# Kernel tuning notes

Measured on AMD Instinct MI355X. Metric: run time of the kernel, lower is better.

## Reference

```python
import jax, jax.numpy as jnp
import numpy as np

TEMPERATURE = 0.1  # base_temperature=0.07 is unused in the original forward
K = 100            # hard-coded top-k in the original forward


def setup_inputs() -> dict:
    key = jax.random.key(0)
    k1, k2, k3, k4 = jax.random.split(key, 4)
    B, T, D, N = 16, 2048, 256, 128
    context_feature = jax.random.normal(k1, (B, T, D), dtype=jnp.float32)
    target_feature = jax.random.normal(k2, (B, T, D), dtype=jnp.float32)
    # torch.unique(mask_index): supply a pre-uniqued sorted 1D index set directly
    mask_index = jnp.sort(jax.random.permutation(k3, T)[:N]).astype(jnp.int32)
    phone_label = jax.random.randint(k4, (B, T), 0, 100, dtype=jnp.int32)
    return {"context_feature": context_feature, "target_feature": target_feature,
            "mask_index": mask_index, "phone_label": phone_label}


def reference(context_feature, target_feature, mask_index, phone_label):
    B, T, D = context_feature.shape
    N = mask_index.shape[0]

    # phone gather + inequality mask (BN, BT)
    phone_n = phone_label[:, mask_index].reshape(B * N)
    phone_t = phone_label.reshape(B * T)
    neq_mask = (phone_n[:, None] != phone_t[None, :]).astype(context_feature.dtype)

    anchors = context_feature[:, mask_index, :].reshape(B * N, D)
    negative = target_feature.reshape(B * T, D)
    positive = target_feature[:, mask_index, :].reshape(B * N, D)

    a_norm = jnp.linalg.norm(anchors, axis=1)   # (BN,)
    p_norm = jnp.linalg.norm(positive, axis=1)  # (BN,)
    n_norm = jnp.linalg.norm(negative, axis=1)  # (BT,)

    # numerator: original builds full (BN,BN) cosine matrix but only uses diag;
    # compute the diagonal directly (identical math, far less memory)
    cos_pos = jnp.sum(anchors * positive, axis=1) / (a_norm * p_norm)
    sim_numerator = jnp.exp(jnp.arccos(jnp.clip(cos_pos, -1.0, 1.0)) / TEMPERATURE)

    # denominator: (BN, BT) cosine -> acos -> exp -> mask -> top-k sum
    cos_neg = (anchors @ negative.T) / (a_norm[:, None] * n_norm[None, :])
    sim_den = jnp.exp(jnp.arccos(jnp.clip(cos_neg, -1.0, 1.0)) / TEMPERATURE) * neq_mask
    top_vals = jax.lax.top_k(sim_den, K)[0]          # == sort desc then take first K
    sim_den_final = top_vals.sum(axis=1)             # (BN,)

    logit = jnp.log(sim_numerator / sim_den_final)
    loss = (-1.0 / (N * B)) * logit.sum()
    return loss
```

## Files before the change

### kernel.cpp

```cpp
#include <hip/hip_runtime.h>
#include <math.h>

#define TT 2048
#define TD 256
#define BN 2048
#define BT 32768
#define KTOP 100
#define CAP 1024
#define LCAP 1024
#define THETA -0.15f
#define BROWS 128
#define SLICE 512
#define NITER 16
#define FSCALE 301.176470588f
#define GH 32

typedef __attribute__((ext_vector_type(8))) short short8v;
typedef __attribute__((ext_vector_type(4))) float float4v;

__device__ __forceinline__ unsigned short f2bf(float f) {
    unsigned u = __float_as_uint(f);
    u += 0x7fffu + ((u >> 16) & 1u);
    return (unsigned short)(u >> 16);
}

__device__ __forceinline__ int tile_off_us(int col, int l) {
    int ks = l >> 3;
    int g = (l >> 1) & 3;
    int e = (l & 1) * 4;
    return ((((col >> 4) * 8 + ks) * 4 + g) * 16 + (col & 15)) * 8 + e;
}

__global__ __launch_bounds__(256) void kinit(const float* __restrict__ ctx,
                                             const float* __restrict__ tgt,
                                             const int* __restrict__ mask_index,
                                             const int* __restrict__ phone,
                                             unsigned short* __restrict__ negT,
                                             unsigned short* __restrict__ ancT,
                                             float* __restrict__ acosP,
                                             int* __restrict__ phoneA,
                                             unsigned* __restrict__ ghp,
                                             int* __restrict__ cnt,
                                             int* __restrict__ flagA) {
    const int bid = blockIdx.x;
    const int tid = threadIdx.x;

    if (bid < 2048) {
        const int col = tid >> 4;
        const int seg = tid & 15;
        const float* src = tgt + ((size_t)bid * 16 + col) * TD + seg * 16;
        float4 v0 = *reinterpret_cast<const float4*>(src + 0);
        float4 v1 = *reinterpret_cast<const float4*>(src + 4);
        float4 v2 = *reinterpret_cast<const float4*>(src + 8);
        float4 v3 = *reinterpret_cast<const float4*>(src + 12);
        float s = v0.x * v0.x + v0.y * v0.y + v0.z * v0.z + v0.w * v0.w
                + v1.x * v1.x + v1.y * v1.y + v1.z * v1.z + v1.w * v1.w
                + v2.x * v2.x + v2.y * v2.y + v2.z * v2.z + v2.w * v2.w
                + v3.x * v3.x + v3.y * v3.y + v3.z * v3.z + v3.w * v3.w;
        s += __shfl_xor(s, 1, 64);
        s += __shfl_xor(s, 2, 64);
        s += __shfl_xor(s, 4, 64);
        s += __shfl_xor(s, 8, 64);
        const float iv = 1.0f / sqrtf(s);
        unsigned short* oa = negT + (size_t)(((bid * 32 + seg * 2) * 16 + col)) * 8;
        unsigned short* ob = oa + 128;
        ushort4 p0, p1, p2, p3;
        p0.x = f2bf(v0.x * iv); p0.y = f2bf(v0.y * iv);
        p0.z = f2bf(v0.z * iv); p0.w = f2bf(v0.w * iv);
        p1.x = f2bf(v1.x * iv); p1.y = f2bf(v1.y * iv);
        p1.z = f2bf(v1.z * iv); p1.w = f2bf(v1.w * iv);
        p2.x = f2bf(v2.x * iv); p2.y = f2bf(v2.y * iv);
        p2.z = f2bf(v2.z * iv); p2.w = f2bf(v2.w * iv);
        p3.x = f2bf(v3.x * iv); p3.y = f2bf(v3.y * iv);
        p3.z = f2bf(v3.z * iv); p3.w = f2bf(v3.w * iv);
        *reinterpret_cast<ushort4*>(oa + 0) = p0;
        *reinterpret_cast<ushort4*>(oa + 4) = p1;
        *reinterpret_cast<ushort4*>(ob + 0) = p2;
        *reinterpret_cast<ushort4*>(ob + 4) = p3;
        return;
    }
    if (bid < 2560) {
        const int r = (bid - 2048) * 4 + (tid >> 6);
        const int lane = tid & 63;
        const int b = r >> 7;
        const int n = r & 127;
        const int t = mask_index[n];
        const size_t base = ((size_t)b * TT + t) * TD;
        float4 a = *reinterpret_cast<const float4*>(ctx + base + lane * 4);
        float4 p = *reinterpret_cast<const float4*>(tgt + base + lane * 4);
        float sa = a.x * a.x + a.y * a.y + a.z * a.z + a.w * a.w;
        float sp = p.x * p.x + p.y * p.y + p.z * p.z + p.w * p.w;
        float dp = a.x * p.x + a.y * p.y + a.z * p.z + a.w * p.w;
        for (int off = 32; off > 0; off >>= 1) {
            sa += __shfl_down(sa, off, 64);
            sp += __shfl_down(sp, off, 64);
            dp += __shfl_down(dp, off, 64);
        }
        sa = __shfl(sa, 0, 64);
        sp = __shfl(sp, 0, 64);
        dp = __shfl(dp, 0, 64);
        const float an = sqrtf(sa);
        const float inva = 1.0f / an;
        if (lane == 0) {
            float cp = dp / (an * sqrtf(sp));
            cp = fminf(1.f, fmaxf(-1.f, cp));
            acosP[r] = acosf(cp) * 10.0f;
            phoneA[r] = phone[b * TT + t];
        }
        ushort4 o;
        o.x = f2bf(a.x * inva); o.y = f2bf(a.y * inva);
        o.z = f2bf(a.z * inva); o.w = f2bf(a.w * inva);
        *reinterpret_cast<ushort4*>(ancT + tile_off_us(r, lane)) = o;
        return;
    }
    if (bid < 2560 + GH) {
        __shared__ unsigned h[128];
        const int s = bid - 2560;
        if (tid < 128) h[tid] = 0u;
        __syncthreads();
        const int base = s * (BT / GH);
        for (int i = tid; i < BT / GH; i += 256)
            atomicAdd(&h[phone[base + i] & 127], 1u);
        __syncthreads();
        if (tid < 128) ghp[s * 128 + tid] = h[tid];
        return;
    }
    {
        const int i = (bid - 2592) * 256 + tid;
        if (i < BN) { cnt[i] = 0; flagA[i] = 0; }
    }
}

__global__ __launch_bounds__(512, 4) void kpass(const short8v* __restrict__ ancT8,
                                                const short8v* __restrict__ negT8,
                                                const int* __restrict__ phoneT,
                                                const int* __restrict__ phoneA,
                                                float* __restrict__ list,
                                                int* __restrict__ cnt,
                                                int* __restrict__ flag) {
    __shared__ float candV[LCAP];
    __shared__ int candR[LCAP];
    __shared__ int s_nc;
    const int tid = threadIdx.x;
    const int w = tid >> 6;
    const int lane = tid & 63;
    const int g = lane >> 4;
    const int c = lane & 15;
    const int wr = w >> 1;
    const int wc = w & 1;
    const int logical = (blockIdx.x & 7) * 128 + (blockIdx.x >> 3);
    const int ct = logical >> 4;
    const int rt = logical & 15;
    const int row0 = rt * BROWS;
    const int colbase = ct * SLICE;

    if (tid == 0) s_nc = 0;

    short8v af[2][8];
#pragma unroll
    for (int mt = 0; mt < 2; ++mt) {
        const int tile = rt * 8 + wr * 2 + mt;
#pragma unroll
        for (int ks = 0; ks < 8; ++ks)
            af[mt][ks] = ancT8[(tile * 8 + ks) * 64 + lane];
    }
    int phA_r[2][4];
#pragma unroll
    for (int mt = 0; mt < 2; ++mt)
#pragma unroll
        for (int j = 0; j < 4; ++j)
            phA_r[mt][j] = phoneA[row0 + wr * 32 + mt * 16 + g * 4 + j];
    __syncthreads();

#pragma unroll 2
    for (int it = 0; it < NITER; ++it) {
        const int cb = colbase + it * 32 + wc * 16;
        const int fb = (cb >> 4) * 512 + lane;
        short8v bf[8];
#pragma unroll
        for (int ks = 0; ks < 8; ++ks)
            bf[ks] = negT8[fb + ks * 64];
        const int ph = phoneT[cb + c];
        float4v acc0 = (float4v){0.f, 0.f, 0.f, 0.f};
        float4v acc1 = (float4v){0.f, 0.f, 0.f, 0.f};
        __builtin_amdgcn_s_setprio(1);
#pragma unroll
        for (int ks = 0; ks < 8; ++ks) {
            acc0 = __builtin_amdgcn_mfma_f32_16x16x32_bf16(af[0][ks], bf[ks], acc0, 0, 0, 0);
            acc1 = __builtin_amdgcn_mfma_f32_16x16x32_bf16(af[1][ks], bf[ks], acc1, 0, 0, 0);
        }
        __builtin_amdgcn_s_setprio(0);
#pragma unroll
        for (int j = 0; j < 4; ++j) {
            float v0 = acc0[j];
            if (v0 < THETA && ph != phA_r[0][j]) {
                int k = atomicAdd(&s_nc, 1);
                if (k < LCAP) {
                    candV[k] = fmaxf(-1.f, v0);
                    candR[k] = row0 + wr * 32 + g * 4 + j;
                }
            }
            float v1 = acc1[j];
            if (v1 < THETA && ph != phA_r[1][j]) {
                int k = atomicAdd(&s_nc, 1);
                if (k < LCAP) {
                    candV[k] = fmaxf(-1.f, v1);
                    candR[k] = row0 + wr * 32 + 16 + g * 4 + j;
                }
            }
        }
    }

    __syncthreads();
    const int nc = s_nc;
    if (nc > LCAP) {
        for (int i = tid; i < BROWS; i += 512) flag[row0 + i] = 1;
    } else {
        for (int i = tid; i < nc; i += 512) {
            const int r = candR[i];
            int idx = atomicAdd(&cnt[r], 1);
            if (idx < CAP) list[(size_t)r * CAP + idx] = candV[i];
        }
    }
}

__global__ __launch_bounds__(64) void kfinal(const float* __restrict__ list,
                                             const int* __restrict__ cnt,
                                             const int* __restrict__ phoneA,
                                             const unsigned* __restrict__ ghp,
                                             const float* __restrict__ acosP,
                                             float* __restrict__ logits,
                                             int* __restrict__ flag) {
    __shared__ float sl[CAP];
    __shared__ unsigned subh[256];
    __shared__ float l2[128];
    __shared__ int s_b, s_cum, s_l2c;
    const int row = blockIdx.x;
    const int lane = threadIdx.x;
    const int mp = phoneA[row] & 127;
    int un = BT;
    for (int s = 0; s < GH; ++s) un -= (int)ghp[s * 128 + mp];
    const int kp = un < KTOP ? un : KTOP;
    const int c = cnt[row];
    if (kp <= 0) { if (lane == 0) logits[row] = acosP[row]; return; }
    if (c < kp || c > CAP) { if (lane == 0) flag[row] = 1; return; }

    for (int i = lane; i < c; i += 64) sl[i] = list[(size_t)row * CAP + i];
    for (int i = lane; i < 256; i += 64) subh[i] = 0u;
    if (lane == 0) s_l2c = 0;
    __syncthreads();

    for (int i = lane; i < c; i += 64) {
        int sb = (int)((sl[i] + 1.0f) * FSCALE);
        sb = sb < 0 ? 0 : (sb > 255 ? 255 : sb);
        atomicAdd(&subh[sb], 1u);
    }
    __syncthreads();
    if (lane == 0) {
        unsigned cum = 0;
        int b = 0;
        for (; b < 256; ++b) {
            if (cum + subh[b] >= (unsigned)kp) break;
            cum += subh[b];
        }
        s_b = b > 255 ? 255 : b;
        s_cum = (int)cum;
    }
    __syncthreads();
    const int bs = s_b, cum = s_cum;

    float ls = 0.f;
    for (int i = lane; i < c; i += 64) {
        float v = sl[i];
        int sb = (int)((v + 1.0f) * FSCALE);
        sb = sb < 0 ? 0 : (sb > 255 ? 255 : sb);
        if (sb < bs) {
            ls += expf(acosf(fminf(1.f, fmaxf(-1.f, v))) * 10.0f);
        } else if (sb == bs) {
            int k = atomicAdd(&s_l2c, 1);
            if (k < 128) l2[k] = v;
        }
    }
#pragma unroll
    for (int off = 1; off < 64; off <<= 1) ls += __shfl_xor(ls, off, 64);
    __syncthreads();
    const int n2 = s_l2c;
    if (n2 > 128) { if (lane == 0) flag[row] = 1; return; }

    float den = ls;
    int rem = kp - cum;
    if (rem > n2) rem = n2;
    float v0 = lane < n2 ? l2[lane] : 1e30f;
    float v1 = lane + 64 < n2 ? l2[lane + 64] : 1e30f;
    for (int it = 0; it < rem; ++it) {
        float mv = fminf(v0, v1);
        int mi = (v1 < v0) ? lane + 64 : lane;
#pragma unroll
        for (int off = 1; off < 64; off <<= 1) {
            float ov = __shfl_xor(mv, off, 64);
            int oi = __shfl_xor(mi, off, 64);
            if (ov < mv || (ov == mv && oi < mi)) { mv = ov; mi = oi; }
        }
        den += expf(acosf(fminf(1.f, fmaxf(-1.f, mv))) * 10.0f);
        if (mi == lane) v0 = 1e30f;
        if (mi == lane + 64) v1 = 1e30f;
    }
    if (lane == 0) logits[row] = acosP[row] - logf(den);
}

__global__ __launch_bounds__(256) void kfallback(const float* __restrict__ ctx,
                                                 const float* __restrict__ tgt,
                                                 const int* __restrict__ mask_index,
                                                 const int* __restrict__ phone,
                                                 const int* __restrict__ flag,
                                                 const unsigned* __restrict__ ghp,
                                                 const float* __restrict__ acosP,
                                                 float* __restrict__ logits) {
    const int row = blockIdx.x;
    if (!flag[row]) return;
    __shared__ float anc[TD];
    __shared__ float redf[256];
    __shared__ int redi[256];
    __shared__ unsigned hist[2048];
    __shared__ float lst[512];
    __shared__ int s_b, s_cum, s_lc;
    const int tid = threadIdx.x;
    const int b = row >> 7;
    const int t = mask_index[row & 127];
    const int mp = phone[b * TT + t];

    {
        float x = ctx[((size_t)b * TT + t) * TD + tid];
        redf[tid] = x * x;
        anc[tid] = x;
        __syncthreads();
        for (int s = 128; s > 0; s >>= 1) {
            if (tid < s) redf[tid] += redf[tid + s];
            __syncthreads();
        }
        float inv = 1.0f / sqrtf(redf[0]);
        __syncthreads();
        anc[tid] *= inv;
    }
    for (int i = tid; i < 2048; i += 256) hist[i] = 0u;
    if (tid == 0) s_lc = 0;
    __syncthreads();

    int un = BT;
    for (int s = 0; s < GH; ++s) un -= (int)ghp[s * 128 + (mp & 127)];
    const int kp = un < KTOP ? un : KTOP;
    if (kp <= 0) { if (tid == 0) logits[row] = acosP[row]; return; }

    for (int col = tid; col < BT; col += 256) {
        if (phone[col] == mp) continue;
        const float* nr = tgt + (size_t)col * TD;
        float dot = 0.f, sq = 0.f;
        for (int d = 0; d < TD; d += 4) {
            float4 v = *reinterpret_cast<const float4*>(nr + d);
            dot += anc[d] * v.x + anc[d + 1] * v.y + anc[d + 2] * v.z + anc[d + 3] * v.w;
            sq += v.x * v.x + v.y * v.y + v.z * v.z + v.w * v.w;
        }
        float cv = fminf(1.f, fmaxf(-1.f, dot / sqrtf(sq)));
        int bb = (int)((cv + 1.0f) * 1024.0f);
        bb = bb > 2047 ? 2047 : bb;
        atomicAdd(&hist[bb], 1u);
    }
    __syncthreads();
    if (tid == 0) {
        unsigned cum = 0;
        int bb = 0;
        for (; bb < 2048; ++bb) {
            if (cum + hist[bb] >= (unsigned)kp) break;
            cum += hist[bb];
        }
        s_b = bb > 2047 ? 2047 : bb;
        s_cum = (int)cum;
    }
    __syncthreads();
    const int bs = s_b;

    float ls = 0.f;
    for (int col = tid; col < BT; col += 256) {
        if (phone[col] == mp) continue;
        const float* nr = tgt + (size_t)col * TD;
        float dot = 0.f, sq = 0.f;
        for (int d = 0; d < TD; d += 4) {
            float4 v = *reinterpret_cast<const float4*>(nr + d);
            dot += anc[d] * v.x + anc[d + 1] * v.y + anc[d + 2] * v.z + anc[d + 3] * v.w;
            sq += v.x * v.x + v.y * v.y + v.z * v.z + v.w * v.w;
        }
        float cv = fminf(1.f, fmaxf(-1.f, dot / sqrtf(sq)));
        int bb = (int)((cv + 1.0f) * 1024.0f);
        bb = bb > 2047 ? 2047 : bb;
        if (bb < bs) {
            ls += expf(acosf(cv) * 10.0f);
        } else if (bb == bs) {
            int k = atomicAdd(&s_lc, 1);
            if (k < 512) lst[k] = cv;
        }
    }
    redf[tid] = ls;
    __syncthreads();
    for (int s = 128; s > 0; s >>= 1) {
        if (tid < s) redf[tid] += redf[tid + s];
        __syncthreads();
    }
    float den = redf[0];
    __syncthreads();

    int lc = s_lc < 512 ? s_lc : 512;
    int rem = kp - s_cum;
    if (rem > lc) rem = lc;
    for (int it = 0; it < rem; ++it) {
        float mv = 1e30f;
        int mi = -1;
        for (int i = tid; i < lc; i += 256) {
            if (lst[i] < mv) { mv = lst[i]; mi = i; }
        }
        redf[tid] = mv;
        redi[tid] = mi;
        __syncthreads();
        for (int s = 128; s > 0; s >>= 1) {
            if (tid < s && (redf[tid + s] < redf[tid] ||
                            (redf[tid + s] == redf[tid] && redi[tid + s] >= 0 &&
                             (redi[tid] < 0 || redi[tid + s] < redi[tid])))) {
                redf[tid] = redf[tid + s];
                redi[tid] = redi[tid + s];
            }
            __syncthreads();
        }
        if (tid == 0) {
            den += expf(acosf(fminf(1.f, fmaxf(-1.f, redf[0]))) * 10.0f);
            if (redi[0] >= 0) lst[redi[0]] = 1e30f;
            redf[0] = den;
        }
        __syncthreads();
        den = redf[0];
        __syncthreads();
    }
    if (tid == 0) logits[row] = acosP[row] - logf(den);
}

__global__ __launch_bounds__(256) void kloss(const float* __restrict__ logits,
                                             float* __restrict__ out) {
    __shared__ float red[256];
    int tid = threadIdx.x;
    float s = 0.f;
    for (int i = tid; i < BN; i += 256) s += logits[i];
    red[tid] = s;
    __syncthreads();
    for (int st = 128; st > 0; st >>= 1) {
        if (tid < st) red[tid] += red[tid + st];
        __syncthreads();
    }
    if (tid == 0) out[0] = -red[0] / (float)BN;
}

extern "C" void kernel_launch(void* const* d_in, const int* in_sizes, int n_in,
                              void* d_out, int out_size, void* d_ws, size_t ws_size,
                              hipStream_t stream) {
    (void)in_sizes; (void)n_in; (void)out_size; (void)ws_size;
    const float* ctx   = (const float*)d_in[0];
    const float* tgt   = (const float*)d_in[1];
    const int*   mask  = (const int*)d_in[2];
    const int*   phone = (const int*)d_in[3];
    float* out = (float*)d_out;

    char* p = (char*)d_ws;
    unsigned short* negT = (unsigned short*)p;            p += (size_t)BT * TD * 2;
    unsigned short* ancT = (unsigned short*)p;            p += (size_t)BN * TD * 2;
    float* acosP  = (float*)p;                            p += (size_t)BN * 4;
    int*   phoneA = (int*)p;                              p += (size_t)BN * 4;
    int*   cntA   = (int*)p;                              p += (size_t)BN * 4;
    int*   flagA  = (int*)p;                              p += (size_t)BN * 4;
    unsigned* ghp = (unsigned*)p;                         p += (size_t)GH * 128 * 4;
    float* listA  = (float*)p;                            p += (size_t)BN * CAP * 4;
    float* logits = (float*)p;                            p += (size_t)BN * 4;

    kinit<<<2600, 256, 0, stream>>>(ctx, tgt, mask, phone, negT, ancT,
                                    acosP, phoneA, ghp, cntA, flagA);
    kpass<<<1024, 512, 0, stream>>>((const short8v*)ancT, (const short8v*)negT,
                                    phone, phoneA, listA, cntA, flagA);
    kfinal<<<BN, 64, 0, stream>>>(listA, cntA, phoneA, ghp, acosP, logits, flagA);
    kfallback<<<BN, 256, 0, stream>>>(ctx, tgt, mask, phone, flagA, ghp, acosP, logits);
    kloss<<<1, 256, 0, stream>>>(logits, out);
}
```

Measured before the change: 134.5 us.

## Widen kpass wave tiles to 64 rows and merge fallback into kfinal

```diff
diff --git a/kernel.cpp b/kernel.cpp
--- a/kernel.cpp
+++ b/kernel.cpp
@@ -11,7 +11,7 @@
 #define THETA -0.15f
 #define BROWS 128
 #define SLICE 512
-#define NITER 16
+#define NITER 8
 #define FSCALE 301.176470588f
 #define GH 32
 
@@ -131,7 +131,7 @@
     }
 }
 
-__global__ __launch_bounds__(512, 4) void kpass(const short8v* __restrict__ ancT8,
+__global__ __launch_bounds__(512, 2) void kpass(const short8v* __restrict__ ancT8,
                                                 const short8v* __restrict__ negT8,
                                                 const int* __restrict__ phoneT,
                                                 const int* __restrict__ phoneA,
@@ -146,8 +146,8 @@
     const int lane = tid & 63;
     const int g = lane >> 4;
     const int c = lane & 15;
-    const int wr = w >> 1;
-    const int wc = w & 1;
+    const int wr = w >> 2;
+    const int wc = w & 3;
     const int logical = (blockIdx.x & 7) * 128 + (blockIdx.x >> 3);
     const int ct = logical >> 4;
     const int rt = logical & 15;
@@ -156,56 +156,55 @@
 
     if (tid == 0) s_nc = 0;
 
-    short8v af[2][8];
-#pragma unroll
-    for (int mt = 0; mt < 2; ++mt) {
-        const int tile = rt * 8 + wr * 2 + mt;
+    short8v af[4][8];
+#pragma unroll
+    for (int mt = 0; mt < 4; ++mt) {
+        const int tile = rt * 8 + wr * 4 + mt;
 #pragma unroll
         for (int ks = 0; ks < 8; ++ks)
             af[mt][ks] = ancT8[(tile * 8 + ks) * 64 + lane];
     }
-    int phA_r[2][4];
-#pragma unroll
-    for (int mt = 0; mt < 2; ++mt)
+    int phA_r[4][4];
+#pragma unroll
+    for (int mt = 0; mt < 4; ++mt)
 #pragma unroll
         for (int j = 0; j < 4; ++j)
-            phA_r[mt][j] = phoneA[row0 + wr * 32 + mt * 16 + g * 4 + j];
+            phA_r[mt][j] = phoneA[row0 + wr * 64 + mt * 16 + g * 4 + j];
     __syncthreads();
 
-#pragma unroll 2
+#pragma unroll 1
     for (int it = 0; it < NITER; ++it) {
-        const int cb = colbase + it * 32 + wc * 16;
+        const int cb = colbase + it * 64 + wc * 16;
         const int fb = (cb >> 4) * 512 + lane;
         short8v bf[8];
 #pragma unroll
         for (int ks = 0; ks < 8; ++ks)
             bf[ks] = negT8[fb + ks * 64];
         const int ph = phoneT[cb + c];
-        float4v acc0 = (float4v){0.f, 0.f, 0.f, 0.f};
-        float4v acc1 = (float4v){0.f, 0.f, 0.f, 0.f};
+        float4v acc[4];
+#pragma unroll
+        for (int mt = 0; mt < 4; ++mt)
+            acc[mt] = (float4v){0.f, 0.f, 0.f, 0.f};
         __builtin_amdgcn_s_setprio(1);
 #pragma unroll
         for (int ks = 0; ks < 8; ++ks) {
-            acc0 = __builtin_amdgcn_mfma_f32_16x16x32_bf16(af[0][ks], bf[ks], acc0, 0, 0, 0);
-            acc1 = __builtin_amdgcn_mfma_f32_16x16x32_bf16(af[1][ks], bf[ks], acc1, 0, 0, 0);
+            acc[0] = __builtin_amdgcn_mfma_f32_16x16x32_bf16(af[0][ks], bf[ks], acc[0], 0, 0, 0);
+            acc[1] = __builtin_amdgcn_mfma_f32_16x16x32_bf16(af[1][ks], bf[ks], acc[1], 0, 0, 0);
+            acc[2] = __builtin_amdgcn_mfma_f32_16x16x32_bf16(af[2][ks], bf[ks], acc[2], 0, 0, 0);
+            acc[3] = __builtin_amdgcn_mfma_f32_16x16x32_bf16(af[3][ks], bf[ks], acc[3], 0, 0, 0);
         }
         __builtin_amdgcn_s_setprio(0);
 #pragma unroll
-        for (int j = 0; j < 4; ++j) {
-            float v0 = acc0[j];
-            if (v0 < THETA && ph != phA_r[0][j]) {
-                int k = atomicAdd(&s_nc, 1);
-                if (k < LCAP) {
-                    candV[k] = fmaxf(-1.f, v0);
-                    candR[k] = row0 + wr * 32 + g * 4 + j;
-                }
-            }
-            float v1 = acc1[j];
-            if (v1 < THETA && ph != phA_r[1][j]) {
-                int k = atomicAdd(&s_nc, 1);
-                if (k < LCAP) {
-                    candV[k] = fmaxf(-1.f, v1);
-                    candR[k] = row0 + wr * 32 + 16 + g * 4 + j;
+        for (int mt = 0; mt < 4; ++mt) {
+#pragma unroll
+            for (int j = 0; j < 4; ++j) {
+                float v = acc[mt][j];
+                if (v < THETA && ph != phA_r[mt][j]) {
+                    int k = atomicAdd(&s_nc, 1);
+                    if (k < LCAP) {
+                        candV[k] = fmaxf(-1.f, v);
+                        candR[k] = row0 + wr * 64 + mt * 16 + g * 4 + j;
+                    }
                 }
             }
         }
@@ -229,11 +228,18 @@
                                              const int* __restrict__ phoneA,
                                              const unsigned* __restrict__ ghp,
                                              const float* __restrict__ acosP,
-                                             float* __restrict__ logits,
-                                             int* __restrict__ flag) {
+                                             const float* __restrict__ ctx,
+                                             const float* __restrict__ tgt,
+                                             const int* __restrict__ mask_index,
+                                             const int* __restrict__ phone,
+                                             const int* __restrict__ flag,
+                                             float* __restrict__ logits) {
     __shared__ float sl[CAP];
     __shared__ unsigned subh[256];
     __shared__ float l2[128];
+    __shared__ float ancS[TD];
+    __shared__ unsigned hist2[2048];
+    __shared__ float lst[512];
     __shared__ int s_b, s_cum, s_l2c;
     const int row = blockIdx.x;
     const int lane = threadIdx.x;
@@ -241,204 +247,169 @@
     int un = BT;
     for (int s = 0; s < GH; ++s) un -= (int)ghp[s * 128 + mp];
     const int kp = un < KTOP ? un : KTOP;
+    if (kp <= 0) { if (lane == 0) logits[row] = acosP[row]; return; }
     const int c = cnt[row];
-    if (kp <= 0) { if (lane == 0) logits[row] = acosP[row]; return; }
-    if (c < kp || c > CAP) { if (lane == 0) flag[row] = 1; return; }
-
-    for (int i = lane; i < c; i += 64) sl[i] = list[(size_t)row * CAP + i];
-    for (int i = lane; i < 256; i += 64) subh[i] = 0u;
-    if (lane == 0) s_l2c = 0;
-    __syncthreads();
-
-    for (int i = lane; i < c; i += 64) {
-        int sb = (int)((sl[i] + 1.0f) * FSCALE);
-        sb = sb < 0 ? 0 : (sb > 255 ? 255 : sb);
-        atomicAdd(&subh[sb], 1u);
-    }
-    __syncthreads();
-    if (lane == 0) {
-        unsigned cum = 0;
-        int b = 0;
-        for (; b < 256; ++b) {
-            if (cum + subh[b] >= (unsigned)kp) break;
-            cum += subh[b];
-        }
-        s_b = b > 255 ? 255 : b;
-        s_cum = (int)cum;
-    }
-    __syncthreads();
-    const int bs = s_b, cum = s_cum;
-
-    float ls = 0.f;
-    for (int i = lane; i < c; i += 64) {
-        float v = sl[i];
-        int sb = (int)((v + 1.0f) * FSCALE);
-        sb = sb < 0 ? 0 : (sb > 255 ? 255 : sb);
-        if (sb < bs) {
-            ls += expf(acosf(fminf(1.f, fmaxf(-1.f, v))) * 10.0f);
-        } else if (sb == bs) {
-            int k = atomicAdd(&s_l2c, 1);
-            if (k < 128) l2[k] = v;
-        }
-    }
-#pragma unroll
-    for (int off = 1; off < 64; off <<= 1) ls += __shfl_xor(ls, off, 64);
-    __syncthreads();
-    const int n2 = s_l2c;
-    if (n2 > 128) { if (lane == 0) flag[row] = 1; return; }
-
-    float den = ls;
-    int rem = kp - cum;
-    if (rem > n2) rem = n2;
-    float v0 = lane < n2 ? l2[lane] : 1e30f;
-    float v1 = lane + 64 < n2 ? l2[lane + 64] : 1e30f;
-    for (int it = 0; it < rem; ++it) {
-        float mv = fminf(v0, v1);
-        int mi = (v1 < v0) ? lane + 64 : lane;
-#pragma unroll
-        for (int off = 1; off < 64; off <<= 1) {
-            float ov = __shfl_xor(mv, off, 64);
-            int oi = __shfl_xor(mi, off, 64);
-            if (ov < mv || (ov == mv && oi < mi)) { mv = ov; mi = oi; }
-        }
-        den += expf(acosf(fminf(1.f, fmaxf(-1.f, mv))) * 10.0f);
-        if (mi == lane) v0 = 1e30f;
-        if (mi == lane + 64) v1 = 1e30f;
-    }
-    if (lane == 0) logits[row] = acosP[row] - logf(den);
-}
-
-__global__ __launch_bounds__(256) void kfallback(const float* __restrict__ ctx,
-                                                 const float* __restrict__ tgt,
-                                                 const int* __restrict__ mask_index,
-                                                 const int* __restrict__ phone,
-                                                 const int* __restrict__ flag,
-                                                 const unsigned* __restrict__ ghp,
-                                                 const float* __restrict__ acosP,
-                                                 float* __restrict__ logits) {
-    const int row = blockIdx.x;
-    if (!flag[row]) return;
-    __shared__ float anc[TD];
-    __shared__ float redf[256];
-    __shared__ int redi[256];
-    __shared__ unsigned hist[2048];
-    __shared__ float lst[512];
-    __shared__ int s_b, s_cum, s_lc;
-    const int tid = threadIdx.x;
-    const int b = row >> 7;
-    const int t = mask_index[row & 127];
-    const int mp = phone[b * TT + t];
+
+    bool fb = (flag[row] != 0) || (c < kp) || (c > CAP);
+    float den = 0.f;
+
+    if (!fb) {
+        for (int i = lane; i < c; i += 64) sl[i] = list[(size_t)row * CAP + i];
+        for (int i = lane; i < 256; i += 64) subh[i] = 0u;
+        if (lane == 0) s_l2c = 0;
+        __syncthreads();
+        for (int i = lane; i < c; i += 64) {
+            int sb = (int)((sl[i] + 1.0f) * FSCALE);
+            sb = sb < 0 ? 0 : (sb > 255 ? 255 : sb);
+            atomicAdd(&subh[sb], 1u);
+        }
+        __syncthreads();
+        if (lane == 0) {
+            unsigned cum = 0;
+            int b = 0;
+            for (; b < 256; ++b) {
+                if (cum + subh[b] >= (unsigned)kp) break;
+                cum += subh[b];
+            }
+            s_b = b > 255 ? 255 : b;
+            s_cum = (int)cum;
+        }
+        __syncthreads();
+        const int bs = s_b, cum = s_cum;
+        float ls = 0.f;
+        for (int i = lane; i < c; i += 64) {
+            float v = sl[i];
+            int sb = (int)((v + 1.0f) * FSCALE);
+            sb = sb < 0 ? 0 : (sb > 255 ? 255 : sb);
+            if (sb < bs) {
+                ls += expf(acosf(fminf(1.f, fmaxf(-1.f, v))) * 10.0f);
+            } else if (sb == bs) {
+                int k = atomicAdd(&s_l2c, 1);
+                if (k < 128) l2[k] = v;
+            }
+        }
+#pragma unroll
+        for (int off = 1; off < 64; off <<= 1) ls += __shfl_xor(ls, off, 64);
+        __syncthreads();
+        const int n2 = s_l2c;
+        if (n2 > 128) {
+            fb = true;
+        } else {
+            den = ls;
+            int rem = kp - cum;
+            if (rem > n2) rem = n2;
+            float v0 = lane < n2 ? l2[lane] : 1e30f;
+            float v1 = lane + 64 < n2 ? l2[lane + 64] : 1e30f;
+            for (int itx = 0; itx < rem; ++itx) {
+                float mv = fminf(v0, v1);
+                int mi = (v1 < v0) ? lane + 64 : lane;
+#pragma unroll
+                for (int off = 1; off < 64; off <<= 1) {
+                    float ov = __shfl_xor(mv, off, 64);
+                    int oi = __shfl_xor(mi, off, 64);
+                    if (ov < mv || (ov == mv && oi < mi)) { mv = ov; mi = oi; }
+                }
+                den += expf(acosf(fminf(1.f, fmaxf(-1.f, mv))) * 10.0f);
+                if (mi == lane) v0 = 1e30f;
+                if (mi == lane + 64) v1 = 1e30f;
+            }
+            if (lane == 0) logits[row] = acosP[row] - logf(den);
+            return;
+        }
+    }
 
     {
-        float x = ctx[((size_t)b * TT + t) * TD + tid];
-        redf[tid] = x * x;
-        anc[tid] = x;
-        __syncthreads();
-        for (int s = 128; s > 0; s >>= 1) {
-            if (tid < s) redf[tid] += redf[tid + s];
+        const int b = row >> 7;
+        const int t = mask_index[row & 127];
+        const int mpf = phone[b * TT + t];
+        float4 a4 = *reinterpret_cast<const float4*>(
+            ctx + ((size_t)b * TT + t) * TD + lane * 4);
+        float sa = a4.x * a4.x + a4.y * a4.y + a4.z * a4.z + a4.w * a4.w;
+#pragma unroll
+        for (int off = 1; off < 64; off <<= 1) sa += __shfl_xor(sa, off, 64);
+        const float inva = 1.0f / sqrtf(sa);
+        ancS[lane * 4 + 0] = a4.x * inva;
+        ancS[lane * 4 + 1] = a4.y * inva;
+        ancS[lane * 4 + 2] = a4.z * inva;
+        ancS[lane * 4 + 3] = a4.w * inva;
+        for (int i = lane; i < 2048; i += 64) hist2[i] = 0u;
+        if (lane == 0) s_l2c = 0;
+        __syncthreads();
+
+        for (int col = lane; col < BT; col += 64) {
+            if (phone[col] == mpf) continue;
+            const float* nr = tgt + (size_t)col * TD;
+            float dot = 0.f, sq = 0.f;
+            for (int d = 0; d < TD; d += 4) {
+                float4 v = *reinterpret_cast<const float4*>(nr + d);
+                dot += ancS[d] * v.x + ancS[d + 1] * v.y + ancS[d + 2] * v.z + ancS[d + 3] * v.w;
+                sq += v.x * v.x + v.y * v.y + v.z * v.z + v.w * v.w;
+            }
+            float cv = fminf(1.f, fmaxf(-1.f, dot / sqrtf(sq)));
+            int bb = (int)((cv + 1.0f) * 1024.0f);
+            bb = bb > 2047 ? 2047 : bb;
+            atomicAdd(&hist2[bb], 1u);
+        }
+        __syncthreads();
+        if (lane == 0) {
+            unsigned cum = 0;
+            int bb = 0;
+            for (; bb < 2048; ++bb) {
+                if (cum + hist2[bb] >= (unsigned)kp) break;
+                cum += hist2[bb];
+            }
+            s_b = bb > 2047 ? 2047 : bb;
+            s_cum = (int)cum;
+        }
+        __syncthreads();
+        const int bs = s_b;
+
+        float ls = 0.f;
+        for (int col = lane; col < BT; col += 64) {
+            if (phone[col] == mpf) continue;
+            const float* nr = tgt + (size_t)col * TD;
+            float dot = 0.f, sq = 0.f;
+            for (int d = 0; d < TD; d += 4) {
+                float4 v = *reinterpret_cast<const float4*>(nr + d);
+                dot += ancS[d] * v.x + ancS[d + 1] * v.y + ancS[d + 2] * v.z + ancS[d + 3] * v.w;
+                sq += v.x * v.x + v.y * v.y + v.z * v.z + v.w * v.w;
+            }
+            float cv = fminf(1.f, fmaxf(-1.f, dot / sqrtf(sq)));
+            int bb = (int)((cv + 1.0f) * 1024.0f);
+            bb = bb > 2047 ? 2047 : bb;
+            if (bb < bs) {
+                ls += expf(acosf(cv) * 10.0f);
+            } else if (bb == bs) {
+                int k = atomicAdd(&s_l2c, 1);
+                if (k < 512) lst[k] = cv;
+            }
+        }
+#pragma unroll
+        for (int off = 1; off < 64; off <<= 1) ls += __shfl_xor(ls, off, 64);
+        __syncthreads();
+        den = ls;
+        int lc = s_l2c < 512 ? s_l2c : 512;
+        int rem = kp - s_cum;
+        if (rem > lc) rem = lc;
+        for (int itx = 0; itx < rem; ++itx) {
+            float mv = 1e30f;
+            int mi = -1;
+            for (int i = lane; i < lc; i += 64) {
+                float x = lst[i];
+                if (x < mv) { mv = x; mi = i; }
+            }
+#pragma unroll
+            for (int off = 1; off < 64; off <<= 1) {
+                float ov = __shfl_xor(mv, off, 64);
+                int oi = __shfl_xor(mi, off, 64);
+                if (ov < mv || (ov == mv && oi >= 0 && (mi < 0 || oi < mi))) { mv = ov; mi = oi; }
+            }
+            den += expf(acosf(fminf(1.f, fmaxf(-1.f, mv))) * 10.0f);
+            if (lane == 0 && mi >= 0) lst[mi] = 1e30f;
             __syncthreads();
         }
-        float inv = 1.0f / sqrtf(redf[0]);
-        __syncthreads();
-        anc[tid] *= inv;
-    }
-    for (int i = tid; i < 2048; i += 256) hist[i] = 0u;
-    if (tid == 0) s_lc = 0;
-    __syncthreads();
-
-    int un = BT;
-    for (int s = 0; s < GH; ++s) un -= (int)ghp[s * 128 + (mp & 127)];
-    const int kp = un < KTOP ? un : KTOP;
-    if (kp <= 0) { if (tid == 0) logits[row] = acosP[row]; return; }
-
-    for (int col = tid; col < BT; col += 256) {
-        if (phone[col] == mp) continue;
-        const float* nr = tgt + (size_t)col * TD;
-        float dot = 0.f, sq = 0.f;
-        for (int d = 0; d < TD; d += 4) {
-            float4 v = *reinterpret_cast<const float4*>(nr + d);
-            dot += anc[d] * v.x + anc[d + 1] * v.y + anc[d + 2] * v.z + anc[d + 3] * v.w;
-            sq += v.x * v.x + v.y * v.y + v.z * v.z + v.w * v.w;
-        }
-        float cv = fminf(1.f, fmaxf(-1.f, dot / sqrtf(sq)));
-        int bb = (int)((cv + 1.0f) * 1024.0f);
-        bb = bb > 2047 ? 2047 : bb;
-        atomicAdd(&hist[bb], 1u);
-    }
-    __syncthreads();
-    if (tid == 0) {
-        unsigned cum = 0;
-        int bb = 0;
-        for (; bb < 2048; ++bb) {
-            if (cum + hist[bb] >= (unsigned)kp) break;
-            cum += hist[bb];
-        }
-        s_b = bb > 2047 ? 2047 : bb;
-        s_cum = (int)cum;
-    }
-    __syncthreads();
-    const int bs = s_b;
-
-    float ls = 0.f;
-    for (int col = tid; col < BT; col += 256) {
-        if (phone[col] == mp) continue;
-        const float* nr = tgt + (size_t)col * TD;
-        float dot = 0.f, sq = 0.f;
-        for (int d = 0; d < TD; d += 4) {
-            float4 v = *reinterpret_cast<const float4*>(nr + d);
-            dot += anc[d] * v.x + anc[d + 1] * v.y + anc[d + 2] * v.z + anc[d + 3] * v.w;
-            sq += v.x * v.x + v.y * v.y + v.z * v.z + v.w * v.w;
-        }
-        float cv = fminf(1.f, fmaxf(-1.f, dot / sqrtf(sq)));
-        int bb = (int)((cv + 1.0f) * 1024.0f);
-        bb = bb > 2047 ? 2047 : bb;
-        if (bb < bs) {
-            ls += expf(acosf(cv) * 10.0f);
-        } else if (bb == bs) {
-            int k = atomicAdd(&s_lc, 1);
-            if (k < 512) lst[k] = cv;
-        }
-    }
-    redf[tid] = ls;
-    __syncthreads();
-    for (int s = 128; s > 0; s >>= 1) {
-        if (tid < s) redf[tid] += redf[tid + s];
-        __syncthreads();
-    }
-    float den = redf[0];
-    __syncthreads();
-
-    int lc = s_lc < 512 ? s_lc : 512;
-    int rem = kp - s_cum;
-    if (rem > lc) rem = lc;
-    for (int it = 0; it < rem; ++it) {
-        float mv = 1e30f;
-        int mi = -1;
-        for (int i = tid; i < lc; i += 256) {
-            if (lst[i] < mv) { mv = lst[i]; mi = i; }
-        }
-        redf[tid] = mv;
-        redi[tid] = mi;
-        __syncthreads();
-        for (int s = 128; s > 0; s >>= 1) {
-            if (tid < s && (redf[tid + s] < redf[tid] ||
-                            (redf[tid + s] == redf[tid] && redi[tid + s] >= 0 &&
-                             (redi[tid] < 0 || redi[tid + s] < redi[tid])))) {
-                redf[tid] = redf[tid + s];
-                redi[tid] = redi[tid + s];
-            }
-            __syncthreads();
-        }
-        if (tid == 0) {
-            den += expf(acosf(fminf(1.f, fmaxf(-1.f, redf[0]))) * 10.0f);
-            if (redi[0] >= 0) lst[redi[0]] = 1e30f;
-            redf[0] = den;
-        }
-        __syncthreads();
-        den = redf[0];
-        __syncthreads();
-    }
-    if (tid == 0) logits[row] = acosP[row] - logf(den);
+        if (lane == 0) logits[row] = acosP[row] - logf(den);
+    }
 }
 
 __global__ __launch_bounds__(256) void kloss(const float* __restrict__ logits,
@@ -481,7 +452,7 @@
                                     acosP, phoneA, ghp, cntA, flagA);
     kpass<<<1024, 512, 0, stream>>>((const short8v*)ancT, (const short8v*)negT,
                                     phone, phoneA, listA, cntA, flagA);
-    kfinal<<<BN, 64, 0, stream>>>(listA, cntA, phoneA, ghp, acosP, logits, flagA);
-    kfallback<<<BN, 256, 0, stream>>>(ctx, tgt, mask, phone, flagA, ghp, acosP, logits);
+    kfinal<<<BN, 64, 0, stream>>>(listA, cntA, phoneA, ghp, acosP,
+                                  ctx, tgt, mask, phone, flagA, logits);
     kloss<<<1, 256, 0, stream>>>(logits, out);
 }
```

Measured after the change: 164.0 us. 21.9% more time.
